# Kernel optimization log

Measured on AMD Instinct MI355X. Metric: run time of the kernel, lower is better.

Reference implementation:

```python
import jax, jax.numpy as jnp
import numpy as np

B, L, D = 32, 128, 512

def setup_inputs() -> dict:
    key = jax.random.key(0)
    ks = jax.random.split(key, 10)
    s = 1.0 / np.sqrt(D)
    return {
        "current_sotw": jax.random.normal(ks[0], (B, L, D), jnp.float32),
        "new_obs": jax.random.normal(ks[1], (B, L, D), jnp.float32),
        "Wq": jax.random.uniform(ks[2], (D, D), jnp.float32, -s, s),   # linear_query weight
        "bq": jax.random.uniform(ks[3], (D,), jnp.float32, -s, s),     # linear_query bias
        "Wc": jax.random.uniform(ks[4], (D, D), jnp.float32, -s, s),   # linear_context (no bias)
        "v": jax.random.uniform(ks[5], (D,), jnp.float32, -s, s),      # v projection to scalar score
        "Wout": jax.random.uniform(ks[6], (2 * D, D), jnp.float32, -s, s),  # linear_out weight
        "bout": jax.random.uniform(ks[7], (D,), jnp.float32, -s, s),        # linear_out bias (mlp type)
        "mix": jax.random.uniform(ks[8], (1,), jnp.float32),           # mixing_proportion ~ U[0,1)
    }

def _global_attn_mlp(source, memory, Wq, bq, Wc, v, Wout, bout):
    # OpenNMT GlobalAttention, attn_type='mlp', attn_func='softmax'
    wq = jnp.einsum('btd,de->bte', source, Wq) + bq          # [B,T,D]
    uh = jnp.einsum('bsd,de->bse', memory, Wc)               # [B,S,D]
    # scores: v . tanh(wq + uh) over broadcast [B,T,S,D]
    scores = jnp.einsum('btsd,d->bts', jnp.tanh(wq[:, :, None, :] + uh[:, None, :, :]), v)
    align = jax.nn.softmax(scores, axis=-1)                  # [B,T,S]
    c = jnp.einsum('bts,bsd->btd', align, memory)            # context [B,T,D]
    attn_h = jnp.einsum('btd,de->bte', jnp.concatenate([c, source], axis=-1), Wout) + bout
    return attn_h  # [B,T,D] (the torch code transposes to [T,B,D] then back)

def reference(current_sotw, new_obs, Wq, bq, Wc, v, Wout, bout, mix):
    a1 = _global_attn_mlp(new_obs, current_sotw, Wq, bq, Wc, v, Wout, bout)
    a2 = _global_attn_mlp(current_sotw, new_obs, Wq, bq, Wc, v, Wout, bout)
    m = mix[0]
    return (1.0 - m) * a1 + m * a2
```

## Files before the change

### kernel.cpp

```cpp
#include <hip/hip_runtime.h>

#define DD 512
#define SS 128
#define TT4 4
#define SCH16 16
#define RW 520
#define C2F 2.8853900817779268f
#define L2EF 1.4426950408889634f

typedef __bf16 bf16x8 __attribute__((ext_vector_type(8)));
typedef float f32x4 __attribute__((ext_vector_type(4)));
typedef unsigned int uint32x4 __attribute__((ext_vector_type(4)));

__device__ __forceinline__ unsigned short f2bf(float f) {
    unsigned int u = __builtin_bit_cast(unsigned int, f);
    u += 0x7fffu + ((u >> 16) & 1u);
    return (unsigned short)(u >> 16);
}
__device__ __forceinline__ float bflo(unsigned int u) { return __builtin_bit_cast(float, u << 16); }
__device__ __forceinline__ float bfhi(unsigned int u) { return __builtin_bit_cast(float, u & 0xffff0000u); }

__global__ __launch_bounds__(256)
void f32_to_bf16_k(const float* __restrict__ in, unsigned short* __restrict__ out, int n8)
{
    int i = blockIdx.x * 256 + threadIdx.x;
    if (i < n8) {
        const float4 a = ((const float4*)in)[2 * i];
        const float4 b = ((const float4*)in)[2 * i + 1];
        uint32x4 o;
        o[0] = (unsigned)f2bf(a.x) | ((unsigned)f2bf(a.y) << 16);
        o[1] = (unsigned)f2bf(a.z) | ((unsigned)f2bf(a.w) << 16);
        o[2] = (unsigned)f2bf(b.x) | ((unsigned)f2bf(b.y) << 16);
        o[3] = (unsigned)f2bf(b.z) | ((unsigned)f2bf(b.w) << 16);
        ((uint32x4*)out)[i] = o;
    }
}

__global__ __launch_bounds__(256)
void transpose_bf16(const float* __restrict__ in, unsigned short* __restrict__ out, int R, int C)
{
    __shared__ float t[64][65];
    const int r0 = blockIdx.y * 64, c0 = blockIdx.x * 64;
    const int tid = threadIdx.x;
    const int lc = tid & 63, lr = tid >> 6;
    #pragma unroll
    for (int i = 0; i < 16; ++i) {
        int r = lr + i * 4;
        t[r][lc] = in[(size_t)(r0 + r) * C + c0 + lc];
    }
    __syncthreads();
    #pragma unroll
    for (int i = 0; i < 16; ++i) {
        int rr = lr + i * 4;
        out[(size_t)(c0 + rr) * R + r0 + lc] = f2bf(t[lc][rr]);
    }
}

__global__ __launch_bounds__(256)
void gemm_proj(const unsigned short* __restrict__ A,
               const unsigned short* __restrict__ Bt,
               const float* __restrict__ bq,
               unsigned short* __restrict__ outW,
               unsigned short* __restrict__ outU)
{
    constexpr int K = 512, LDA = 72;
    __shared__ __align__(16) unsigned short As[64][LDA];
    __shared__ __align__(16) unsigned short Bs[64][LDA];

    const int tid = threadIdx.x;
    const int n0 = blockIdx.x * 64, m0 = blockIdx.y * 64;
    const int lane = tid & 63, wid = tid >> 6;
    const int wr = wid >> 1, wc = wid & 1;
    const int lr = lane & 15, kb = lane >> 4;

    f32x4 acc[2][2] = {};
    uint32x4 ra[2], rb[2];

    auto LOADK = [&](int k0) {
        #pragma unroll
        for (int j = 0; j < 2; ++j) {
            int id = tid + 256 * j; int r = id >> 3, s = id & 7;
            ra[j] = *(const uint32x4*)&A[(size_t)(m0 + r) * K + k0 + s * 8];
            rb[j] = *(const uint32x4*)&Bt[(size_t)(n0 + r) * K + k0 + s * 8];
        }
    };

    LOADK(0);
    #pragma unroll 1
    for (int step = 0; step < K / 64; ++step) {
        __syncthreads();
        #pragma unroll
        for (int j = 0; j < 2; ++j) {
            int id = tid + 256 * j; int r = id >> 3, s = id & 7;
            *(uint32x4*)&As[r][s * 8] = ra[j];
            *(uint32x4*)&Bs[r][s * 8] = rb[j];
        }
        __syncthreads();
        if (step + 1 < K / 64) LOADK((step + 1) * 64);
        #pragma unroll
        for (int kk = 0; kk < 64; kk += 32) {
            bf16x8 b0 = __builtin_bit_cast(bf16x8, *(const uint32x4*)&Bs[wc * 32 + lr][kk + kb * 8]);
            bf16x8 b1 = __builtin_bit_cast(bf16x8, *(const uint32x4*)&Bs[wc * 32 + 16 + lr][kk + kb * 8]);
            #pragma unroll
            for (int mf = 0; mf < 2; ++mf) {
                bf16x8 a0 = __builtin_bit_cast(bf16x8, *(const uint32x4*)&As[wr * 32 + mf * 16 + lr][kk + kb * 8]);
                acc[mf][0] = __builtin_amdgcn_mfma_f32_16x16x32_bf16(a0, b0, acc[mf][0], 0, 0, 0);
                acc[mf][1] = __builtin_amdgcn_mfma_f32_16x16x32_bf16(a0, b1, acc[mf][1], 0, 0, 0);
            }
        }
    }

    #pragma unroll
    for (int nf = 0; nf < 2; ++nf) {
        const int col = n0 + wc * 32 + nf * 16 + lr;
        #pragma unroll
        for (int mf = 0; mf < 2; ++mf) {
            const int row = m0 + wr * 32 + mf * 16 + kb * 4;
            #pragma unroll
            for (int r = 0; r < 4; ++r) {
                const float valf = acc[mf][nf][r];
                if (col < 512) outW[(size_t)(row + r) * 512 + col] = f2bf((valf + bq[col]) * C2F);
                else           outU[(size_t)(row + r) * 512 + (col - 512)] = f2bf(valf);
            }
        }
    }
}

__global__ __launch_bounds__(256)
void gemm_final(const unsigned short* __restrict__ c1, const unsigned short* __restrict__ c2,
                const float* __restrict__ no, const float* __restrict__ cs,
                const float* __restrict__ mix,
                const unsigned short* __restrict__ Bt,
                const float* __restrict__ bout, float* __restrict__ out)
{
    constexpr int K = 1024, LDA = 72;
    __shared__ __align__(16) unsigned short As[64][LDA];
    __shared__ __align__(16) unsigned short Bs[64][LDA];

    const int tid = threadIdx.x;
    const int n0 = blockIdx.x * 64, m0 = blockIdx.y * 64;
    const int lane = tid & 63, wid = tid >> 6;
    const int wr = wid >> 1, wc = wid & 1;
    const int lr = lane & 15, kb = lane >> 4;
    const float mxv = mix[0], omv = 1.0f - mxv;

    f32x4 acc[2][2] = {};
    uint32x4 ra[2], rb[2];

    auto LOADK = [&](int k0) {
        #pragma unroll
        for (int j = 0; j < 2; ++j) {
            int id = tid + 256 * j; int r = id >> 3, s = id & 7;
            const size_t row = m0 + r;
            const int k = k0 + s * 8;
            uint32x4 o;
            if (k < 512) {
                const uint32x4 x1 = *(const uint32x4*)&c1[row * 512 + k];
                const uint32x4 x2 = *(const uint32x4*)&c2[row * 512 + k];
                #pragma unroll
                for (int q = 0; q < 4; ++q) {
                    float lo = omv * bflo(x1[q]) + mxv * bflo(x2[q]);
                    float hi = omv * bfhi(x1[q]) + mxv * bfhi(x2[q]);
                    o[q] = (unsigned)f2bf(lo) | ((unsigned)f2bf(hi) << 16);
                }
            } else {
                const float* n1 = &no[row * 512 + k - 512];
                const float* s1 = &cs[row * 512 + k - 512];
                const float4 a1 = *(const float4*)n1, a2 = *(const float4*)(n1 + 4);
                const float4 b1 = *(const float4*)s1, b2 = *(const float4*)(s1 + 4);
                o[0] = (unsigned)f2bf(omv * a1.x + mxv * b1.x) | ((unsigned)f2bf(omv * a1.y + mxv * b1.y) << 16);
                o[1] = (unsigned)f2bf(omv * a1.z + mxv * b1.z) | ((unsigned)f2bf(omv * a1.w + mxv * b1.w) << 16);
                o[2] = (unsigned)f2bf(omv * a2.x + mxv * b2.x) | ((unsigned)f2bf(omv * a2.y + mxv * b2.y) << 16);
                o[3] = (unsigned)f2bf(omv * a2.z + mxv * b2.z) | ((unsigned)f2bf(omv * a2.w + mxv * b2.w) << 16);
            }
            ra[j] = o;
            rb[j] = *(const uint32x4*)&Bt[(size_t)(n0 + r) * K + k0 + s * 8];
        }
    };

    LOADK(0);
    #pragma unroll 1
    for (int step = 0; step < K / 64; ++step) {
        __syncthreads();
        #pragma unroll
        for (int j = 0; j < 2; ++j) {
            int id = tid + 256 * j; int r = id >> 3, s = id & 7;
            *(uint32x4*)&As[r][s * 8] = ra[j];
            *(uint32x4*)&Bs[r][s * 8] = rb[j];
        }
        __syncthreads();
        if (step + 1 < K / 64) LOADK((step + 1) * 64);
        #pragma unroll
        for (int kk = 0; kk < 64; kk += 32) {
            bf16x8 b0 = __builtin_bit_cast(bf16x8, *(const uint32x4*)&Bs[wc * 32 + lr][kk + kb * 8]);
            bf16x8 b1 = __builtin_bit_cast(bf16x8, *(const uint32x4*)&Bs[wc * 32 + 16 + lr][kk + kb * 8]);
            #pragma unroll
            for (int mf = 0; mf < 2; ++mf) {
                bf16x8 a0 = __builtin_bit_cast(bf16x8, *(const uint32x4*)&As[wr * 32 + mf * 16 + lr][kk + kb * 8]);
                acc[mf][0] = __builtin_amdgcn_mfma_f32_16x16x32_bf16(a0, b0, acc[mf][0], 0, 0, 0);
                acc[mf][1] = __builtin_amdgcn_mfma_f32_16x16x32_bf16(a0, b1, acc[mf][1], 0, 0, 0);
            }
        }
    }

    #pragma unroll
    for (int nf = 0; nf < 2; ++nf) {
        const int col = n0 + wc * 32 + nf * 16 + lr;
        const float bv = bout[col];
        #pragma unroll
        for (int mf = 0; mf < 2; ++mf) {
            const int row = m0 + wr * 32 + mf * 16 + kb * 4;
            #pragma unroll
            for (int r = 0; r < 4; ++r)
                out[(size_t)(row + r) * 512 + col] = acc[mf][nf][r] + bv;
        }
    }
}

__global__ __launch_bounds__(512, 8)
void attn_fused(const unsigned short* __restrict__ wq,
                const unsigned short* __restrict__ uh,
                const float* __restrict__ v,
                const unsigned short* __restrict__ mem,
                unsigned short* __restrict__ c_out)
{
    __shared__ __align__(16) unsigned short s_wq[TT4 * RW];
    __shared__ __align__(16) unsigned short s_uh[SCH16 * RW];
    __shared__ __align__(16) float s_v2[DD];
    __shared__ float s_sc[TT4 * SS];

    const int b = blockIdx.y, t0 = blockIdx.x * TT4;
    const int tid = threadIdx.x;

    if (tid < 256) {
        const int row = tid >> 6, G = tid & 63;
        const int P = ((G & 7) << 3) | (G >> 3);
        *(uint32x4*)&s_wq[row * RW + P * 8] =
            *(const uint32x4*)&wq[((size_t)b * SS + t0 + row) * DD + G * 8];
    } else if (tid < 384) {
        const int H = tid - 256;
        const int P = ((H & 15) << 3) | (H >> 4);
        float4 val = *(const float4*)&v[H * 4];
        val.x *= 2.f; val.y *= 2.f; val.z *= 2.f; val.w *= 2.f;
        *(float4*)&s_v2[P * 4] = val;
    }

    const int oct = tid & 7;
    const int sr  = (tid >> 3) & 15;
    const int t   = tid >> 7;

    for (int sc0 = 0; sc0 < SS; sc0 += SCH16) {
        __syncthreads();
        {
            int i = tid;
            #pragma unroll
            for (int rep = 0; rep < 2; ++rep, i += 512) {
                const int row = i >> 6, G = i & 63;
                const int P = ((G & 7) << 3) | (G >> 3);
                *(uint32x4*)&s_uh[row * RW + P * 8] =
                    *(const uint32x4*)&uh[((size_t)b * SS + sc0 + row) * DD + G * 8];
            }
        }
        __syncthreads();

        const unsigned short* wrow = &s_wq[t * RW];
        const unsigned short* urow = &s_uh[sr * RW];

        float a0 = 0.f, a1 = 0.f, a2 = 0.f, a3 = 0.f;
        #pragma unroll 4
        for (int j = 0; j < 8; ++j) {
            const uint32x4 w4 = *(const uint32x4*)&wrow[(8 * j + oct) * 8];
            const uint32x4 u4 = *(const uint32x4*)&urow[(8 * j + oct) * 8];
            const float4 vA = *(const float4*)&s_v2[(16 * j + oct) * 4];
            const float4 vB = *(const float4*)&s_v2[(16 * j + 8 + oct) * 4];
            float x, e;
            x = fmaf(C2F, bflo(u4[0]), bflo(w4[0])); e = __builtin_amdgcn_exp2f(x);
            a0 = fmaf(vA.x, __builtin_amdgcn_rcpf(e + 1.f), a0);
            x = fmaf(C2F, bfhi(u4[0]), bfhi(w4[0])); e = __builtin_amdgcn_exp2f(x);
            a1 = fmaf(vA.y, __builtin_amdgcn_rcpf(e + 1.f), a1);
            x = fmaf(C2F, bflo(u4[1]), bflo(w4[1])); e = __builtin_amdgcn_exp2f(x);
            a2 = fmaf(vA.z, __builtin_amdgcn_rcpf(e + 1.f), a2);
            x = fmaf(C2F, bfhi(u4[1]), bfhi(w4[1])); e = __builtin_amdgcn_exp2f(x);
            a3 = fmaf(vA.w, __builtin_amdgcn_rcpf(e + 1.f), a3);
            x = fmaf(C2F, bflo(u4[2]), bflo(w4[2])); e = __builtin_amdgcn_exp2f(x);
            a0 = fmaf(vB.x, __builtin_amdgcn_rcpf(e + 1.f), a0);
            x = fmaf(C2F, bfhi(u4[2]), bfhi(w4[2])); e = __builtin_amdgcn_exp2f(x);
            a1 = fmaf(vB.y, __builtin_amdgcn_rcpf(e + 1.f), a1);
            x = fmaf(C2F, bflo(u4[3]), bflo(w4[3])); e = __builtin_amdgcn_exp2f(x);
            a2 = fmaf(vB.z, __builtin_amdgcn_rcpf(e + 1.f), a2);
            x = fmaf(C2F, bfhi(u4[3]), bfhi(w4[3])); e = __builtin_amdgcn_exp2f(x);
            a3 = fmaf(vB.w, __builtin_amdgcn_rcpf(e + 1.f), a3);
        }
        float p = (a0 + a1) + (a2 + a3);
        p += __shfl_xor(p, 1);
        p += __shfl_xor(p, 2);
        p += __shfl_xor(p, 4);
        if (oct == 0) s_sc[t * SS + sc0 + sr] = -p;
    }
    __syncthreads();

    if (tid < 128) {
        const int tr = tid >> 5, l32 = tid & 31;
        float x0 = s_sc[tr * SS + l32];
        float x1 = s_sc[tr * SS + l32 + 32];
        float x2 = s_sc[tr * SS + l32 + 64];
        float x3 = s_sc[tr * SS + l32 + 96];
        float mx = fmaxf(fmaxf(x0, x1), fmaxf(x2, x3));
        #pragma unroll
        for (int off = 16; off > 0; off >>= 1) mx = fmaxf(mx, __shfl_xor(mx, off));
        const float e0 = __builtin_amdgcn_exp2f((x0 - mx) * L2EF);
        const float e1 = __builtin_amdgcn_exp2f((x1 - mx) * L2EF);
        const float e2 = __builtin_amdgcn_exp2f((x2 - mx) * L2EF);
        const float e3 = __builtin_amdgcn_exp2f((x3 - mx) * L2EF);
        float sum = (e0 + e1) + (e2 + e3);
        #pragma unroll
        for (int off = 16; off > 0; off >>= 1) sum += __shfl_xor(sum, off);
        const float rs = __builtin_amdgcn_rcpf(sum);
        s_sc[tr * SS + l32]      = e0 * rs;
        s_sc[tr * SS + l32 + 32] = e1 * rs;
        s_sc[tr * SS + l32 + 64] = e2 * rs;
        s_sc[tr * SS + l32 + 96] = e3 * rs;
    }

    const int w = tid >> 6, lane = tid & 63;
    const int tb = w & 3, half = w >> 2;
    const int d = half * 256 + lane * 4;
    f32x4 ac = {0.f, 0.f, 0.f, 0.f};

    for (int sc0 = 0; sc0 < SS; sc0 += SCH16) {
        __syncthreads();
        {
            int i = tid;
            #pragma unroll
            for (int rep = 0; rep < 2; ++rep, i += 512) {
                const int row = i >> 6, G = i & 63;
                *(uint32x4*)&s_uh[row * RW + G * 8] =
                    *(const uint32x4*)&mem[((size_t)b * SS + sc0 + row) * DD + G * 8];
            }
        }
        __syncthreads();
        #pragma unroll
        for (int srow = 0; srow < SCH16; ++srow) {
            const float e = s_sc[tb * SS + sc0 + srow];
            const uint2 mv = *(const uint2*)&s_uh[srow * RW + d];
            ac[0] = fmaf(e, bflo(mv.x), ac[0]);
            ac[1] = fmaf(e, bfhi(mv.x), ac[1]);
            ac[2] = fmaf(e, bflo(mv.y), ac[2]);
            ac[3] = fmaf(e, bfhi(mv.y), ac[3]);
        }
    }
    uint2 st;
    st.x = (unsigned)f2bf(ac[0]) | ((unsigned)f2bf(ac[1]) << 16);
    st.y = (unsigned)f2bf(ac[2]) | ((unsigned)f2bf(ac[3]) << 16);
    *(uint2*)&c_out[((size_t)b * SS + t0 + tb) * DD + d] = st;
}

extern "C" void kernel_launch(void* const* d_in, const int* in_sizes, int n_in,
                              void* d_out, int out_size, void* d_ws, size_t ws_size,
                              hipStream_t stream) {
    const float* cs   = (const float*)d_in[0];
    const float* no   = (const float*)d_in[1];
    const float* Wq   = (const float*)d_in[2];
    const float* bq   = (const float*)d_in[3];
    const float* Wc   = (const float*)d_in[4];
    const float* v    = (const float*)d_in[5];
    const float* Wout = (const float*)d_in[6];
    const float* bout = (const float*)d_in[7];
    const float* mix  = (const float*)d_in[8];
    float* out = (float*)d_out;

    typedef unsigned short us;
    char* ws = (char*)d_ws;
    us* cs_bf = (us*)(ws);
    us* no_bf = (us*)(ws + (4u  << 20));
    us* Wqct  = (us*)(ws + (8u  << 20));
    us* Woutt = (us*)(ws + (9u  << 20));
    us* wq1   = (us*)(ws + (10u << 20));
    us* uh2   = (us*)(ws + (14u << 20));
    us* wq2   = (us*)(ws + (18u << 20));
    us* uh1   = (us*)(ws + (22u << 20));
    us* c1    = (us*)(ws + (26u << 20));
    us* c2    = (us*)(ws + (10u << 20));

    const dim3 b256(256);
    const int n8 = 4096 * DD / 8;

    f32_to_bf16_k<<<dim3(n8 / 256), b256, 0, stream>>>(cs, cs_bf, n8);
    f32_to_bf16_k<<<dim3(n8 / 256), b256, 0, stream>>>(no, no_bf, n8);
    transpose_bf16<<<dim3(8, 8),  b256, 0, stream>>>(Wq, Wqct, 512, 512);
    transpose_bf16<<<dim3(8, 8),  b256, 0, stream>>>(Wc, Wqct + 512 * 512, 512, 512);
    transpose_bf16<<<dim3(8, 16), b256, 0, stream>>>(Wout, Woutt, 1024, 512);

    gemm_proj<<<dim3(16, 64), b256, 0, stream>>>(no_bf, Wqct, bq, wq1, uh2);
    gemm_proj<<<dim3(16, 64), b256, 0, stream>>>(cs_bf, Wqct, bq, wq2, uh1);

    attn_fused<<<dim3(32, 32), dim3(512), 0, stream>>>(wq1, uh1, v, cs_bf, c1);
    attn_fused<<<dim3(32, 32), dim3(512), 0, stream>>>(wq2, uh2, v, no_bf, c2);

    gemm_final<<<dim3(8, 64), b256, 0, stream>>>(c1, c2, no, cs, mix, Woutt, bout, out);
}
```

Measured before the change: 333.5 us.

## Merge prep kernels, enlarge GEMM M-tiles, store v as bf16 in attention

Merges the two f32-to-bf16 conversions into one launch and the three weight transposes into one launch. Folds both projection GEMMs into a single launch using blockIdx.z. Doubles the M tile of the projection and output GEMMs to 128 rows for more reuse of the B tile. In the attention kernel, drops the permuted shared-memory layout and stores v as bf16 to cut LDS traffic, at some precision cost and possible new bank conflicts.

```diff
diff --git a/kernel.cpp b/kernel.cpp
--- a/kernel.cpp
+++ b/kernel.cpp
@@ -21,32 +21,41 @@
 __device__ __forceinline__ float bfhi(unsigned int u) { return __builtin_bit_cast(float, u & 0xffff0000u); }
 
 __global__ __launch_bounds__(256)
-void f32_to_bf16_k(const float* __restrict__ in, unsigned short* __restrict__ out, int n8)
+void cvt_dual(const float* __restrict__ a, const float* __restrict__ b,
+              unsigned short* __restrict__ oa, unsigned short* __restrict__ ob, int n8)
 {
     int i = blockIdx.x * 256 + threadIdx.x;
-    if (i < n8) {
-        const float4 a = ((const float4*)in)[2 * i];
-        const float4 b = ((const float4*)in)[2 * i + 1];
-        uint32x4 o;
-        o[0] = (unsigned)f2bf(a.x) | ((unsigned)f2bf(a.y) << 16);
-        o[1] = (unsigned)f2bf(a.z) | ((unsigned)f2bf(a.w) << 16);
-        o[2] = (unsigned)f2bf(b.x) | ((unsigned)f2bf(b.y) << 16);
-        o[3] = (unsigned)f2bf(b.z) | ((unsigned)f2bf(b.w) << 16);
-        ((uint32x4*)out)[i] = o;
-    }
+    const float* in; unsigned short* out; int k;
+    if (i < n8) { in = a; out = oa; k = i; }
+    else        { in = b; out = ob; k = i - n8; }
+    const float4 x = ((const float4*)in)[2 * k];
+    const float4 y = ((const float4*)in)[2 * k + 1];
+    uint32x4 o;
+    o[0] = (unsigned)f2bf(x.x) | ((unsigned)f2bf(x.y) << 16);
+    o[1] = (unsigned)f2bf(x.z) | ((unsigned)f2bf(x.w) << 16);
+    o[2] = (unsigned)f2bf(y.x) | ((unsigned)f2bf(y.y) << 16);
+    o[3] = (unsigned)f2bf(y.z) | ((unsigned)f2bf(y.w) << 16);
+    ((uint32x4*)out)[k] = o;
 }
 
 __global__ __launch_bounds__(256)
-void transpose_bf16(const float* __restrict__ in, unsigned short* __restrict__ out, int R, int C)
+void transpose_all(const float* __restrict__ Wq, const float* __restrict__ Wc,
+                   const float* __restrict__ Wout,
+                   unsigned short* __restrict__ Wqct, unsigned short* __restrict__ Woutt)
 {
     __shared__ float t[64][65];
-    const int r0 = blockIdx.y * 64, c0 = blockIdx.x * 64;
+    const int z = blockIdx.z;
+    const float* in; unsigned short* out; int R, r0;
+    if (z == 0)      { in = Wq;   out = Wqct;             R = 512;  r0 = blockIdx.y * 64; }
+    else if (z == 1) { in = Wc;   out = Wqct + 512 * 512; R = 512;  r0 = blockIdx.y * 64; }
+    else             { in = Wout; out = Woutt;            R = 1024; r0 = (z - 2) * 512 + blockIdx.y * 64; }
+    const int c0 = blockIdx.x * 64;
     const int tid = threadIdx.x;
     const int lc = tid & 63, lr = tid >> 6;
     #pragma unroll
     for (int i = 0; i < 16; ++i) {
         int r = lr + i * 4;
-        t[r][lc] = in[(size_t)(r0 + r) * C + c0 + lc];
+        t[r][lc] = in[(size_t)(r0 + r) * 512 + c0 + lc];
     }
     __syncthreads();
     #pragma unroll
@@ -57,30 +66,37 @@
 }
 
 __global__ __launch_bounds__(256)
-void gemm_proj(const unsigned short* __restrict__ A,
-               const unsigned short* __restrict__ Bt,
-               const float* __restrict__ bq,
-               unsigned short* __restrict__ outW,
-               unsigned short* __restrict__ outU)
+void gemm_proj(const unsigned short* __restrict__ A0, const unsigned short* __restrict__ A1,
+               const unsigned short* __restrict__ Bt, const float* __restrict__ bq,
+               unsigned short* __restrict__ w0, unsigned short* __restrict__ u0,
+               unsigned short* __restrict__ w1, unsigned short* __restrict__ u1)
 {
     constexpr int K = 512, LDA = 72;
-    __shared__ __align__(16) unsigned short As[64][LDA];
+    __shared__ __align__(16) unsigned short As[128][LDA];
     __shared__ __align__(16) unsigned short Bs[64][LDA];
 
+    const unsigned short* A = blockIdx.z ? A1 : A0;
+    unsigned short* outW    = blockIdx.z ? w1 : w0;
+    unsigned short* outU    = blockIdx.z ? u1 : u0;
+
     const int tid = threadIdx.x;
-    const int n0 = blockIdx.x * 64, m0 = blockIdx.y * 64;
+    const int n0 = blockIdx.x * 64, m0 = blockIdx.y * 128;
     const int lane = tid & 63, wid = tid >> 6;
     const int wr = wid >> 1, wc = wid & 1;
     const int lr = lane & 15, kb = lane >> 4;
 
-    f32x4 acc[2][2] = {};
-    uint32x4 ra[2], rb[2];
+    f32x4 acc[4][2] = {};
+    uint32x4 ra[4], rb[2];
 
     auto LOADK = [&](int k0) {
         #pragma unroll
+        for (int j = 0; j < 4; ++j) {
+            int id = tid + 256 * j; int r = id >> 3, s = id & 7;
+            ra[j] = *(const uint32x4*)&A[(size_t)(m0 + r) * K + k0 + s * 8];
+        }
+        #pragma unroll
         for (int j = 0; j < 2; ++j) {
             int id = tid + 256 * j; int r = id >> 3, s = id & 7;
-            ra[j] = *(const uint32x4*)&A[(size_t)(m0 + r) * K + k0 + s * 8];
             rb[j] = *(const uint32x4*)&Bt[(size_t)(n0 + r) * K + k0 + s * 8];
         }
     };
@@ -90,9 +106,13 @@
     for (int step = 0; step < K / 64; ++step) {
         __syncthreads();
         #pragma unroll
+        for (int j = 0; j < 4; ++j) {
+            int id = tid + 256 * j; int r = id >> 3, s = id & 7;
+            *(uint32x4*)&As[r][s * 8] = ra[j];
+        }
+        #pragma unroll
         for (int j = 0; j < 2; ++j) {
             int id = tid + 256 * j; int r = id >> 3, s = id & 7;
-            *(uint32x4*)&As[r][s * 8] = ra[j];
             *(uint32x4*)&Bs[r][s * 8] = rb[j];
         }
         __syncthreads();
@@ -102,8 +122,8 @@
             bf16x8 b0 = __builtin_bit_cast(bf16x8, *(const uint32x4*)&Bs[wc * 32 + lr][kk + kb * 8]);
             bf16x8 b1 = __builtin_bit_cast(bf16x8, *(const uint32x4*)&Bs[wc * 32 + 16 + lr][kk + kb * 8]);
             #pragma unroll
-            for (int mf = 0; mf < 2; ++mf) {
-                bf16x8 a0 = __builtin_bit_cast(bf16x8, *(const uint32x4*)&As[wr * 32 + mf * 16 + lr][kk + kb * 8]);
+            for (int mf = 0; mf < 4; ++mf) {
+                bf16x8 a0 = __builtin_bit_cast(bf16x8, *(const uint32x4*)&As[wr * 64 + mf * 16 + lr][kk + kb * 8]);
                 acc[mf][0] = __builtin_amdgcn_mfma_f32_16x16x32_bf16(a0, b0, acc[mf][0], 0, 0, 0);
                 acc[mf][1] = __builtin_amdgcn_mfma_f32_16x16x32_bf16(a0, b1, acc[mf][1], 0, 0, 0);
             }
@@ -113,13 +133,14 @@
     #pragma unroll
     for (int nf = 0; nf < 2; ++nf) {
         const int col = n0 + wc * 32 + nf * 16 + lr;
-        #pragma unroll
-        for (int mf = 0; mf < 2; ++mf) {
-            const int row = m0 + wr * 32 + mf * 16 + kb * 4;
+        const float bv = (col < 512) ? bq[col] : 0.0f;
+        #pragma unroll
+        for (int mf = 0; mf < 4; ++mf) {
+            const int row = m0 + wr * 64 + mf * 16 + kb * 4;
             #pragma unroll
             for (int r = 0; r < 4; ++r) {
                 const float valf = acc[mf][nf][r];
-                if (col < 512) outW[(size_t)(row + r) * 512 + col] = f2bf((valf + bq[col]) * C2F);
+                if (col < 512) outW[(size_t)(row + r) * 512 + col] = f2bf((valf + bv) * C2F);
                 else           outU[(size_t)(row + r) * 512 + (col - 512)] = f2bf(valf);
             }
         }
@@ -129,27 +150,26 @@
 __global__ __launch_bounds__(256)
 void gemm_final(const unsigned short* __restrict__ c1, const unsigned short* __restrict__ c2,
                 const float* __restrict__ no, const float* __restrict__ cs,
-                const float* __restrict__ mix,
-                const unsigned short* __restrict__ Bt,
+                const float* __restrict__ mix, const unsigned short* __restrict__ Bt,
                 const float* __restrict__ bout, float* __restrict__ out)
 {
     constexpr int K = 1024, LDA = 72;
-    __shared__ __align__(16) unsigned short As[64][LDA];
+    __shared__ __align__(16) unsigned short As[128][LDA];
     __shared__ __align__(16) unsigned short Bs[64][LDA];
 
     const int tid = threadIdx.x;
-    const int n0 = blockIdx.x * 64, m0 = blockIdx.y * 64;
+    const int n0 = blockIdx.x * 64, m0 = blockIdx.y * 128;
     const int lane = tid & 63, wid = tid >> 6;
     const int wr = wid >> 1, wc = wid & 1;
     const int lr = lane & 15, kb = lane >> 4;
     const float mxv = mix[0], omv = 1.0f - mxv;
 
-    f32x4 acc[2][2] = {};
-    uint32x4 ra[2], rb[2];
+    f32x4 acc[4][2] = {};
+    uint32x4 ra[4], rb[2];
 
     auto LOADK = [&](int k0) {
         #pragma unroll
-        for (int j = 0; j < 2; ++j) {
+        for (int j = 0; j < 4; ++j) {
             int id = tid + 256 * j; int r = id >> 3, s = id & 7;
             const size_t row = m0 + r;
             const int k = k0 + s * 8;
@@ -174,6 +194,10 @@
                 o[3] = (unsigned)f2bf(omv * a2.z + mxv * b2.z) | ((unsigned)f2bf(omv * a2.w + mxv * b2.w) << 16);
             }
             ra[j] = o;
+        }
+        #pragma unroll
+        for (int j = 0; j < 2; ++j) {
+            int id = tid + 256 * j; int r = id >> 3, s = id & 7;
             rb[j] = *(const uint32x4*)&Bt[(size_t)(n0 + r) * K + k0 + s * 8];
         }
     };
@@ -183,9 +207,13 @@
     for (int step = 0; step < K / 64; ++step) {
         __syncthreads();
         #pragma unroll
+        for (int j = 0; j < 4; ++j) {
+            int id = tid + 256 * j; int r = id >> 3, s = id & 7;
+            *(uint32x4*)&As[r][s * 8] = ra[j];
+        }
+        #pragma unroll
         for (int j = 0; j < 2; ++j) {
             int id = tid + 256 * j; int r = id >> 3, s = id & 7;
-            *(uint32x4*)&As[r][s * 8] = ra[j];
             *(uint32x4*)&Bs[r][s * 8] = rb[j];
         }
         __syncthreads();
@@ -195,8 +223,8 @@
             bf16x8 b0 = __builtin_bit_cast(bf16x8, *(const uint32x4*)&Bs[wc * 32 + lr][kk + kb * 8]);
             bf16x8 b1 = __builtin_bit_cast(bf16x8, *(const uint32x4*)&Bs[wc * 32 + 16 + lr][kk + kb * 8]);
             #pragma unroll
-            for (int mf = 0; mf < 2; ++mf) {
-                bf16x8 a0 = __builtin_bit_cast(bf16x8, *(const uint32x4*)&As[wr * 32 + mf * 16 + lr][kk + kb * 8]);
+            for (int mf = 0; mf < 4; ++mf) {
+                bf16x8 a0 = __builtin_bit_cast(bf16x8, *(const uint32x4*)&As[wr * 64 + mf * 16 + lr][kk + kb * 8]);
                 acc[mf][0] = __builtin_amdgcn_mfma_f32_16x16x32_bf16(a0, b0, acc[mf][0], 0, 0, 0);
                 acc[mf][1] = __builtin_amdgcn_mfma_f32_16x16x32_bf16(a0, b1, acc[mf][1], 0, 0, 0);
             }
@@ -208,8 +236,8 @@
         const int col = n0 + wc * 32 + nf * 16 + lr;
         const float bv = bout[col];
         #pragma unroll
-        for (int mf = 0; mf < 2; ++mf) {
-            const int row = m0 + wr * 32 + mf * 16 + kb * 4;
+        for (int mf = 0; mf < 4; ++mf) {
+            const int row = m0 + wr * 64 + mf * 16 + kb * 4;
             #pragma unroll
             for (int r = 0; r < 4; ++r)
                 out[(size_t)(row + r) * 512 + col] = acc[mf][nf][r] + bv;
@@ -226,7 +254,7 @@
 {
     __shared__ __align__(16) unsigned short s_wq[TT4 * RW];
     __shared__ __align__(16) unsigned short s_uh[SCH16 * RW];
-    __shared__ __align__(16) float s_v2[DD];
+    __shared__ __align__(16) unsigned short s_v2[DD];
     __shared__ float s_sc[TT4 * SS];
 
     const int b = blockIdx.y, t0 = blockIdx.x * TT4;
@@ -234,15 +262,18 @@
 
     if (tid < 256) {
         const int row = tid >> 6, G = tid & 63;
-        const int P = ((G & 7) << 3) | (G >> 3);
-        *(uint32x4*)&s_wq[row * RW + P * 8] =
+        *(uint32x4*)&s_wq[row * RW + G * 8] =
             *(const uint32x4*)&wq[((size_t)b * SS + t0 + row) * DD + G * 8];
-    } else if (tid < 384) {
+    } else if (tid < 320) {
         const int H = tid - 256;
-        const int P = ((H & 15) << 3) | (H >> 4);
-        float4 val = *(const float4*)&v[H * 4];
-        val.x *= 2.f; val.y *= 2.f; val.z *= 2.f; val.w *= 2.f;
-        *(float4*)&s_v2[P * 4] = val;
+        const float4 p = *(const float4*)&v[H * 8];
+        const float4 q = *(const float4*)&v[H * 8 + 4];
+        uint32x4 o;
+        o[0] = (unsigned)f2bf(p.x * 2.f) | ((unsigned)f2bf(p.y * 2.f) << 16);
+        o[1] = (unsigned)f2bf(p.z * 2.f) | ((unsigned)f2bf(p.w * 2.f) << 16);
+        o[2] = (unsigned)f2bf(q.x * 2.f) | ((unsigned)f2bf(q.y * 2.f) << 16);
+        o[3] = (unsigned)f2bf(q.z * 2.f) | ((unsigned)f2bf(q.w * 2.f) << 16);
+        *(uint32x4*)&s_v2[H * 8] = o;
     }
 
     const int oct = tid & 7;
@@ -256,8 +287,7 @@
             #pragma unroll
             for (int rep = 0; rep < 2; ++rep, i += 512) {
                 const int row = i >> 6, G = i & 63;
-                const int P = ((G & 7) << 3) | (G >> 3);
-                *(uint32x4*)&s_uh[row * RW + P * 8] =
+                *(uint32x4*)&s_uh[row * RW + G * 8] =
                     *(const uint32x4*)&uh[((size_t)b * SS + sc0 + row) * DD + G * 8];
             }
         }
@@ -267,29 +297,29 @@
         const unsigned short* urow = &s_uh[sr * RW];
 
         float a0 = 0.f, a1 = 0.f, a2 = 0.f, a3 = 0.f;
-        #pragma unroll 4
+        #pragma unroll
         for (int j = 0; j < 8; ++j) {
-            const uint32x4 w4 = *(const uint32x4*)&wrow[(8 * j + oct) * 8];
-            const uint32x4 u4 = *(const uint32x4*)&urow[(8 * j + oct) * 8];
-            const float4 vA = *(const float4*)&s_v2[(16 * j + oct) * 4];
-            const float4 vB = *(const float4*)&s_v2[(16 * j + 8 + oct) * 4];
+            const int ch = (8 * j + oct) * 8;
+            const uint32x4 w4 = *(const uint32x4*)&wrow[ch];
+            const uint32x4 u4 = *(const uint32x4*)&urow[ch];
+            const uint32x4 v4 = *(const uint32x4*)&s_v2[ch];
             float x, e;
             x = fmaf(C2F, bflo(u4[0]), bflo(w4[0])); e = __builtin_amdgcn_exp2f(x);
-            a0 = fmaf(vA.x, __builtin_amdgcn_rcpf(e + 1.f), a0);
+            a0 = fmaf(bflo(v4[0]), __builtin_amdgcn_rcpf(e + 1.f), a0);
             x = fmaf(C2F, bfhi(u4[0]), bfhi(w4[0])); e = __builtin_amdgcn_exp2f(x);
-            a1 = fmaf(vA.y, __builtin_amdgcn_rcpf(e + 1.f), a1);
+            a1 = fmaf(bfhi(v4[0]), __builtin_amdgcn_rcpf(e + 1.f), a1);
             x = fmaf(C2F, bflo(u4[1]), bflo(w4[1])); e = __builtin_amdgcn_exp2f(x);
-            a2 = fmaf(vA.z, __builtin_amdgcn_rcpf(e + 1.f), a2);
+            a2 = fmaf(bflo(v4[1]), __builtin_amdgcn_rcpf(e + 1.f), a2);
             x = fmaf(C2F, bfhi(u4[1]), bfhi(w4[1])); e = __builtin_amdgcn_exp2f(x);
-            a3 = fmaf(vA.w, __builtin_amdgcn_rcpf(e + 1.f), a3);
+            a3 = fmaf(bfhi(v4[1]), __builtin_amdgcn_rcpf(e + 1.f), a3);
             x = fmaf(C2F, bflo(u4[2]), bflo(w4[2])); e = __builtin_amdgcn_exp2f(x);
-            a0 = fmaf(vB.x, __builtin_amdgcn_rcpf(e + 1.f), a0);
+            a0 = fmaf(bflo(v4[2]), __builtin_amdgcn_rcpf(e + 1.f), a0);
             x = fmaf(C2F, bfhi(u4[2]), bfhi(w4[2])); e = __builtin_amdgcn_exp2f(x);
-            a1 = fmaf(vB.y, __builtin_amdgcn_rcpf(e + 1.f), a1);
+            a1 = fmaf(bfhi(v4[2]), __builtin_amdgcn_rcpf(e + 1.f), a1);
             x = fmaf(C2F, bflo(u4[3]), bflo(w4[3])); e = __builtin_amdgcn_exp2f(x);
-            a2 = fmaf(vB.z, __builtin_amdgcn_rcpf(e + 1.f), a2);
+            a2 = fmaf(bflo(v4[3]), __builtin_amdgcn_rcpf(e + 1.f), a2);
             x = fmaf(C2F, bfhi(u4[3]), bfhi(w4[3])); e = __builtin_amdgcn_exp2f(x);
-            a3 = fmaf(vB.w, __builtin_amdgcn_rcpf(e + 1.f), a3);
+            a3 = fmaf(bfhi(v4[3]), __builtin_amdgcn_rcpf(e + 1.f), a3);
         }
         float p = (a0 + a1) + (a2 + a3);
         p += __shfl_xor(p, 1);
@@ -385,17 +415,14 @@
     const dim3 b256(256);
     const int n8 = 4096 * DD / 8;
 
-    f32_to_bf16_k<<<dim3(n8 / 256), b256, 0, stream>>>(cs, cs_bf, n8);
-    f32_to_bf16_k<<<dim3(n8 / 256), b256, 0, stream>>>(no, no_bf, n8);
-    transpose_bf16<<<dim3(8, 8),  b256, 0, stream>>>(Wq, Wqct, 512, 512);
-    transpose_bf16<<<dim3(8, 8),  b256, 0, stream>>>(Wc, Wqct + 512 * 512, 512, 512);
-    transpose_bf16<<<dim3(8, 16), b256, 0, stream>>>(Wout, Woutt, 1024, 512);
-
-    gemm_proj<<<dim3(16, 64), b256, 0, stream>>>(no_bf, Wqct, bq, wq1, uh2);
-    gemm_proj<<<dim3(16, 64), b256, 0, stream>>>(cs_bf, Wqct, bq, wq2, uh1);
+    cvt_dual<<<dim3(2 * n8 / 256), b256, 0, stream>>>(cs, no, cs_bf, no_bf, n8);
+    transpose_all<<<dim3(8, 8, 4), b256, 0, stream>>>(Wq, Wc, Wout, Wqct, Woutt);
+
+    gemm_proj<<<dim3(16, 32, 2), b256, 0, stream>>>(no_bf, cs_bf, Wqct, bq,
+                                                    wq1, uh2, wq2, uh1);
 
     attn_fused<<<dim3(32, 32), dim3(512), 0, stream>>>(wq1, uh1, v, cs_bf, c1);
     attn_fused<<<dim3(32, 32), dim3(512), 0, stream>>>(wq2, uh2, v, no_bf, c2);
 
-    gemm_final<<<dim3(8, 64), b256, 0, stream>>>(c1, c2, no, cs, mix, Woutt, bout, out);
-}
+    gemm_final<<<dim3(8, 32), b256, 0, stream>>>(c1, c2, no, cs, mix, Woutt, bout, out);
+}
```

After: 337.0 us. No clear change (+1.0%).
